# Performance work log

Hardware: AMD Instinct MI355X
Metric: run time of the kernel (lower is better)

Reference implementation:

```python
import jax, jax.numpy as jnp
import numpy as np

EPS = 1e-8  # matches PairwiseCosine eps clamp


def setup_inputs() -> dict:
    key = jax.random.key(0)
    k1, k2, k3 = jax.random.split(key, 3)
    B, N, M, D = 8, 2048, 2048, 256
    desc_src = jax.random.normal(k1, (B, N, D), dtype=jnp.float32)
    desc_dst = jax.random.normal(k2, (B, M, D), dtype=jnp.float32)
    points_dst = jax.random.uniform(k3, (B, M, 2), dtype=jnp.float32)
    return {"desc_src": desc_src, "desc_dst": desc_dst, "points_dst": points_dst}


def reference(desc_src, desc_dst, points_dst):
    # Pairwise cosine similarity: [B, N, M]
    xx = jnp.linalg.norm(desc_src, axis=-1, keepdims=True)          # [B, N, 1]
    yy = jnp.linalg.norm(desc_dst, axis=-1, keepdims=True)          # [B, M, 1]
    xy = jnp.einsum('bnd,bmd->bnm', desc_src, desc_dst)             # [B, N, M]
    sim = xy / jnp.maximum(xx * jnp.swapaxes(yy, 1, 2), EPS)
    # Best match per source descriptor
    confidence = jnp.max(sim, axis=2)                               # [B, N]
    idx = jnp.argmax(sim, axis=2)                                   # [B, N]
    # Gather matched destination points: [B, N, 2]
    matched = jnp.take_along_axis(points_dst, idx[:, :, None], axis=1)
    return (matched, confidence)
```

## Files before the change

kernel.cpp:

```cpp
#include <hip/hip_runtime.h>
#include <stdint.h>

constexpr int Bq = 8, Nq = 2048, Mq = 2048, Dq = 256;
constexpr int TILE = 128;
constexpr int KC = 32;
constexpr int NCH = Dq / KC;
constexpr int LDS_S = 40;

typedef float f32x4 __attribute__((ext_vector_type(4)));
typedef _Float16 f16x8 __attribute__((ext_vector_type(8)));
typedef __fp16 fp16x2 __attribute__((ext_vector_type(2)));

__device__ __forceinline__ uint32_t f2sortable(float f) {
  uint32_t u = __float_as_uint(f);
  return (u & 0x80000000u) ? ~u : (u | 0x80000000u);
}
__device__ __forceinline__ float sortable2f(uint32_t s) {
  uint32_t u = (s & 0x80000000u) ? (s ^ 0x80000000u) : ~s;
  return __uint_as_float(u);
}

__device__ __forceinline__ void load16(float* d, const float* __restrict__ p) {
  *(float4*)&d[0]  = *(const float4*)(p + 0);
  *(float4*)&d[4]  = *(const float4*)(p + 4);
  *(float4*)&d[8]  = *(const float4*)(p + 8);
  *(float4*)&d[12] = *(const float4*)(p + 12);
}

__device__ __forceinline__ void split8(const float* x, f16x8* hi, f16x8* lo,
                                       float& sq) {
  union { f16x8 v; fp16x2 p[4]; } H, L;
#pragma unroll
  for (int j = 0; j < 4; ++j) {
    float x0 = x[2 * j], x1 = x[2 * j + 1];
    sq = fmaf(x0, x0, sq);
    sq = fmaf(x1, x1, sq);
    float h0 = __uint_as_float(__float_as_uint(x0) & 0xFFFFE000u);
    float h1 = __uint_as_float(__float_as_uint(x1) & 0xFFFFE000u);
    H.p[j] = __builtin_amdgcn_cvt_pkrtz(h0, h1);
    L.p[j] = __builtin_amdgcn_cvt_pkrtz(x0 - h0, x1 - h1);
  }
  *hi = H.v;
  *lo = L.v;
}

__global__ __launch_bounds__(256, 3)
void simmax_kernel(const float* __restrict__ src, const float* __restrict__ dst,
                   unsigned long long* __restrict__ best) {
  __shared__ _Float16 Ah[TILE][LDS_S], Al[TILE][LDS_S];
  __shared__ _Float16 Bh[TILE][LDS_S], Bl[TILE][LDS_S];
  __shared__ float invnx_s[TILE], invny_s[TILE];

  const int b = blockIdx.z, nt = blockIdx.y, mt = blockIdx.x;
  const int tid = threadIdx.x;
  const int lane = tid & 63;
  const int wave = tid >> 6;
  const int wy = wave >> 1, wx = wave & 1;
  const int ln15 = lane & 15, lq = lane >> 4;

  const int sr = tid >> 1;
  const int sk = (tid & 1) * 16;
  const float* Ag = src + ((size_t)(b * Nq + nt * TILE + sr)) * Dq + sk;
  const float* Bg = dst + ((size_t)(b * Mq + mt * TILE + sr)) * Dq + sk;

  f32x4 acc[4][4];
#pragma unroll
  for (int i = 0; i < 4; ++i)
#pragma unroll
    for (int j = 0; j < 4; ++j) acc[i][j] = (f32x4){0.f, 0.f, 0.f, 0.f};
  float sqa = 0.f, sqb = 0.f;

  float av[16], bv[16];
  load16(av, Ag);
  load16(bv, Bg);

  for (int c = 0; c < NCH; ++c) {
    f16x8 ah2[2], al2[2], bh2[2], bl2[2];
    split8(&av[0], &ah2[0], &al2[0], sqa);
    split8(&av[8], &ah2[1], &al2[1], sqa);
    split8(&bv[0], &bh2[0], &bl2[0], sqb);
    split8(&bv[8], &bh2[1], &bl2[1], sqb);
    __syncthreads();
    *(f16x8*)&Ah[sr][sk]     = ah2[0];
    *(f16x8*)&Ah[sr][sk + 8] = ah2[1];
    *(f16x8*)&Al[sr][sk]     = al2[0];
    *(f16x8*)&Al[sr][sk + 8] = al2[1];
    *(f16x8*)&Bh[sr][sk]     = bh2[0];
    *(f16x8*)&Bh[sr][sk + 8] = bh2[1];
    *(f16x8*)&Bl[sr][sk]     = bl2[0];
    *(f16x8*)&Bl[sr][sk + 8] = bl2[1];
    __syncthreads();

    if (c + 1 < NCH) {
      load16(av, Ag + (c + 1) * KC);
      load16(bv, Bg + (c + 1) * KC);
    }

    f16x8 bhf[4], blf[4];
#pragma unroll
    for (int ct = 0; ct < 4; ++ct) {
      int rowb = wx * 64 + ct * 16 + ln15;
      bhf[ct] = *(const f16x8*)&Bh[rowb][lq * 8];
      blf[ct] = *(const f16x8*)&Bl[rowb][lq * 8];
    }
#pragma unroll
    for (int rt = 0; rt < 4; ++rt) {
      int rowa = wy * 64 + rt * 16 + ln15;
      f16x8 ahf = *(const f16x8*)&Ah[rowa][lq * 8];
      f16x8 alf = *(const f16x8*)&Al[rowa][lq * 8];
#pragma unroll
      for (int ct = 0; ct < 4; ++ct) {
        acc[rt][ct] = __builtin_amdgcn_mfma_f32_16x16x32_f16(ahf, bhf[ct], acc[rt][ct], 0, 0, 0);
        acc[rt][ct] = __builtin_amdgcn_mfma_f32_16x16x32_f16(ahf, blf[ct], acc[rt][ct], 0, 0, 0);
        acc[rt][ct] = __builtin_amdgcn_mfma_f32_16x16x32_f16(alf, bhf[ct], acc[rt][ct], 0, 0, 0);
      }
    }
  }

  sqa += __shfl_xor(sqa, 1);
  sqb += __shfl_xor(sqb, 1);
  if ((tid & 1) == 0) {
    invnx_s[sr] = 1.0f / sqrtf(sqa);
    invny_s[sr] = 1.0f / sqrtf(sqb);
  }
  __syncthreads();

  float invny[4];
#pragma unroll
  for (int ct = 0; ct < 4; ++ct) invny[ct] = invny_s[wx * 64 + ct * 16 + ln15];

#pragma unroll
  for (int rt = 0; rt < 4; ++rt) {
#pragma unroll
    for (int reg = 0; reg < 4; ++reg) {
      float bq = -1e30f;
      int bc = 0x7FFFFFFF;
#pragma unroll
      for (int ct = 0; ct < 4; ++ct) {
        float q = acc[rt][ct][reg] * invny[ct];
        int cg = mt * TILE + wx * 64 + ct * 16 + ln15;
        if (q > bq || (q == bq && cg < bc)) { bq = q; bc = cg; }
      }
#pragma unroll
      for (int m = 1; m <= 8; m <<= 1) {
        float q2 = __shfl_xor(bq, m);
        int c2 = __shfl_xor(bc, m);
        if (q2 > bq || (q2 == bq && c2 < bc)) { bq = q2; bc = c2; }
      }
      if (ln15 == 0) {
        int rloc = wy * 64 + rt * 16 + lq * 4 + reg;
        float conf = bq * invnx_s[rloc];
        unsigned long long p =
            ((unsigned long long)(f2sortable(conf) ^ 0x80000000u) << 32) |
            (uint32_t)(~(uint32_t)bc);
        atomicMax((long long*)&best[(size_t)b * Nq + nt * TILE + rloc],
                  (long long)p);
      }
    }
  }
}

__global__ void finalize_kernel(const unsigned long long* __restrict__ best,
                                const float* __restrict__ pts,
                                float* __restrict__ out) {
  int i = blockIdx.x * blockDim.x + threadIdx.x;
  if (i >= Bq * Nq) return;
  unsigned long long p = best[i];
  uint32_t s = (uint32_t)(p >> 32) ^ 0x80000000u;
  int idx = (int)(~(uint32_t)(p & 0xFFFFFFFFull));
  float conf = sortable2f(s);
  int b = i / Nq;
  const float* q = pts + ((size_t)b * Mq + (size_t)idx) * 2;
  out[(size_t)i * 2 + 0] = q[0];
  out[(size_t)i * 2 + 1] = q[1];
  out[(size_t)(Bq * Nq) * 2 + i] = conf;
}

extern "C" void kernel_launch(void* const* d_in, const int* in_sizes, int n_in,
                              void* d_out, int out_size, void* d_ws, size_t ws_size,
                              hipStream_t stream) {
  const float* src = (const float*)d_in[0];
  const float* dst = (const float*)d_in[1];
  const float* pts = (const float*)d_in[2];
  float* out = (float*)d_out;

  unsigned long long* best = (unsigned long long*)d_ws;

  {
    dim3 grid(Mq / TILE, Nq / TILE, Bq);
    simmax_kernel<<<grid, 256, 0, stream>>>(src, dst, best);
  }
  {
    int blocks = (Bq * Nq + 255) / 256;
    finalize_kernel<<<blocks, 256, 0, stream>>>(best, pts, out);
  }
}
```

Measured before the change: 149.1 us.

## Precompute fp16 hi/lo splits and norms in a prep pass, stage via global_load_lds

Adds a prep kernel that splits src and dst into fp16 hi/lo halves, computes inverse norms, and writes them in a chunk-major layout. The main MFMA kernel then streams the pre-split tiles straight into double-buffered LDS with global_load_lds, so each tile no longer repeats the split and the sync-heavy register-to-LDS store. This costs an extra kernel launch and a round trip of the fp16 workspace through memory, and the fast path only runs when the workspace is large enough.

```diff
diff --git a/kernel.cpp b/kernel.cpp
--- a/kernel.cpp
+++ b/kernel.cpp
@@ -9,6 +9,7 @@
 
 typedef float f32x4 __attribute__((ext_vector_type(4)));
 typedef _Float16 f16x8 __attribute__((ext_vector_type(8)));
+typedef _Float16 f16x4 __attribute__((ext_vector_type(4)));
 typedef __fp16 fp16x2 __attribute__((ext_vector_type(2)));
 
 __device__ __forceinline__ uint32_t f2sortable(float f) {
@@ -42,6 +43,151 @@
   }
   *hi = H.v;
   *lo = L.v;
+}
+
+
+__global__ __launch_bounds__(256)
+void prep_kernel(const float* __restrict__ src, const float* __restrict__ dst,
+                 _Float16* __restrict__ Ah, _Float16* __restrict__ Al,
+                 _Float16* __restrict__ Bh, _Float16* __restrict__ Bl,
+                 float* __restrict__ invnx, float* __restrict__ invny) {
+  const int lane = threadIdx.x & 63;
+  const int wv = threadIdx.x >> 6;
+  const int r = blockIdx.x * 4 + wv;
+
+  const float* x;
+  _Float16 *h, *l;
+  float* inv;
+  if (blockIdx.y == 0) { x = src; h = Ah; l = Al; inv = invnx; }
+  else                 { x = dst; h = Bh; l = Bl; inv = invny; }
+
+  float4 v = *(const float4*)(x + (size_t)r * Dq + lane * 4);
+  float sq = 0.f;
+  union { f16x4 v; fp16x2 p[2]; } H, L;
+  float e[4] = {v.x, v.y, v.z, v.w};
+#pragma unroll
+  for (int j = 0; j < 2; ++j) {
+    float x0 = e[2 * j], x1 = e[2 * j + 1];
+    sq = fmaf(x0, x0, sq);
+    sq = fmaf(x1, x1, sq);
+    float h0 = __uint_as_float(__float_as_uint(x0) & 0xFFFFE000u);
+    float h1 = __uint_as_float(__float_as_uint(x1) & 0xFFFFE000u);
+    H.p[j] = __builtin_amdgcn_cvt_pkrtz(h0, h1);
+    L.p[j] = __builtin_amdgcn_cvt_pkrtz(x0 - h0, x1 - h1);
+  }
+#pragma unroll
+  for (int m = 1; m <= 32; m <<= 1) sq += __shfl_xor(sq, m);
+
+  const int b = r >> 11, row = r & 2047;
+  const int c = lane >> 3, ko = (lane & 7) * 4;
+  size_t idx = ((size_t)(b * NCH + c) * 2048 + row) * KC + ko;
+  *(f16x4*)&h[idx] = H.v;
+  *(f16x4*)&l[idx] = L.v;
+  if (lane == 0) inv[r] = 1.0f / sqrtf(sq);
+}
+
+__device__ __forceinline__ void stage(const _Float16* g, _Float16* l, int lane) {
+  const char* gc = (const char*)g + lane * 16;
+  char* lc = (char*)l;
+#pragma unroll
+  for (int i = 0; i < 8; ++i)
+    __builtin_amdgcn_global_load_lds(
+        (const __attribute__((address_space(1))) void*)(gc + i * 1024),
+        (__attribute__((address_space(3))) void*)(lc + i * 1024),
+        16, 0, 0);
+}
+
+__global__ __launch_bounds__(256, 2)
+void simmax_mfma(const _Float16* __restrict__ Ah, const _Float16* __restrict__ Al,
+                 const _Float16* __restrict__ Bh, const _Float16* __restrict__ Bl,
+                 const float* __restrict__ invnx, const float* __restrict__ invny,
+                 unsigned long long* __restrict__ best) {
+  __shared__ __align__(16) _Float16 lds[2][4][TILE][KC];
+
+  const int b = blockIdx.z, nt = blockIdx.y, mt = blockIdx.x;
+  const int tid = threadIdx.x;
+  const int lane = tid & 63;
+  const int wave = tid >> 6;
+  const int wy = wave >> 1, wx = wave & 1;
+  const int ln15 = lane & 15, lq = lane >> 4;
+
+  const _Float16* garr = (wave == 0) ? Ah : (wave == 1) ? Al
+                        : (wave == 2) ? Bh : Bl;
+  const int grow = ((wave < 2) ? nt : mt) * TILE;
+  const _Float16* g0 = garr + ((size_t)(b * NCH) * 2048 + grow) * KC;
+  constexpr size_t CSTR = (size_t)2048 * KC;
+
+  f32x4 acc[4][4];
+#pragma unroll
+  for (int i = 0; i < 4; ++i)
+#pragma unroll
+    for (int j = 0; j < 4; ++j) acc[i][j] = (f32x4){0.f, 0.f, 0.f, 0.f};
+
+  stage(g0, &lds[0][wave][0][0], lane);
+  __syncthreads();
+
+#pragma unroll
+  for (int c = 0; c < NCH; ++c) {
+    const int cb = c & 1;
+    if (c + 1 < NCH)
+      stage(g0 + (size_t)(c + 1) * CSTR, &lds[cb ^ 1][wave][0][0], lane);
+
+    f16x8 bhf[4], blf[4];
+#pragma unroll
+    for (int ct = 0; ct < 4; ++ct) {
+      const int rb = wx * 64 + ct * 16 + ln15;
+      bhf[ct] = *(const f16x8*)&lds[cb][2][rb][lq * 8];
+      blf[ct] = *(const f16x8*)&lds[cb][3][rb][lq * 8];
+    }
+#pragma unroll
+    for (int rt = 0; rt < 4; ++rt) {
+      const int ra = wy * 64 + rt * 16 + ln15;
+      f16x8 ahf = *(const f16x8*)&lds[cb][0][ra][lq * 8];
+      f16x8 alf = *(const f16x8*)&lds[cb][1][ra][lq * 8];
+#pragma unroll
+      for (int ct = 0; ct < 4; ++ct) {
+        acc[rt][ct] = __builtin_amdgcn_mfma_f32_16x16x32_f16(ahf, bhf[ct], acc[rt][ct], 0, 0, 0);
+        acc[rt][ct] = __builtin_amdgcn_mfma_f32_16x16x32_f16(ahf, blf[ct], acc[rt][ct], 0, 0, 0);
+        acc[rt][ct] = __builtin_amdgcn_mfma_f32_16x16x32_f16(alf, bhf[ct], acc[rt][ct], 0, 0, 0);
+      }
+    }
+    if (c + 1 < NCH) __syncthreads();
+  }
+
+  float invy[4];
+#pragma unroll
+  for (int ct = 0; ct < 4; ++ct)
+    invy[ct] = invny[(size_t)b * Mq + mt * TILE + wx * 64 + ct * 16 + ln15];
+
+#pragma unroll
+  for (int rt = 0; rt < 4; ++rt) {
+#pragma unroll
+    for (int reg = 0; reg < 4; ++reg) {
+      float bq = -1e30f;
+      int bc = 0x7FFFFFFF;
+#pragma unroll
+      for (int ct = 0; ct < 4; ++ct) {
+        float q = acc[rt][ct][reg] * invy[ct];
+        int cg = mt * TILE + wx * 64 + ct * 16 + ln15;
+        if (q > bq || (q == bq && cg < bc)) { bq = q; bc = cg; }
+      }
+#pragma unroll
+      for (int m = 1; m <= 8; m <<= 1) {
+        float q2 = __shfl_xor(bq, m);
+        int c2 = __shfl_xor(bc, m);
+        if (q2 > bq || (q2 == bq && c2 < bc)) { bq = q2; bc = c2; }
+      }
+      if (ln15 == 0) {
+        int rloc = wy * 64 + rt * 16 + lq * 4 + reg;
+        float conf = bq * invnx[(size_t)b * Nq + nt * TILE + rloc];
+        unsigned long long p =
+            ((unsigned long long)(f2sortable(conf) ^ 0x80000000u) << 32) |
+            (uint32_t)(~(uint32_t)bc);
+        atomicMax((long long*)&best[(size_t)b * Nq + nt * TILE + rloc],
+                  (long long)p);
+      }
+    }
+  }
 }
 
 __global__ __launch_bounds__(256, 3)
@@ -186,9 +332,27 @@
 
   unsigned long long* best = (unsigned long long*)d_ws;
 
-  {
-    dim3 grid(Mq / TILE, Nq / TILE, Bq);
-    simmax_kernel<<<grid, 256, 0, stream>>>(src, dst, best);
+  constexpr size_t BEST_B = (size_t)Bq * Nq * 8;
+  constexpr size_t HL_B   = (size_t)Bq * 2048 * Dq * 2;
+  constexpr size_t INV_B  = (size_t)Bq * 2048 * 4;
+  constexpr size_t NEED   = BEST_B + 4 * HL_B + 2 * INV_B;
+
+  if (ws_size >= NEED) {
+    uint8_t* w = (uint8_t*)d_ws + BEST_B;
+    _Float16* Ah = (_Float16*)(w);
+    _Float16* Al = (_Float16*)(w + 1 * HL_B);
+    _Float16* Bh = (_Float16*)(w + 2 * HL_B);
+    _Float16* Bl = (_Float16*)(w + 3 * HL_B);
+    float* invnx = (float*)(w + 4 * HL_B);
+    float* invny = (float*)(w + 4 * HL_B + INV_B);
+
+    prep_kernel<<<dim3(4096, 2, 1), 256, 0, stream>>>(src, dst, Ah, Al, Bh, Bl,
+                                                      invnx, invny);
+    simmax_mfma<<<dim3(Mq / TILE, Nq / TILE, Bq), 256, 0, stream>>>(
+        Ah, Al, Bh, Bl, invnx, invny, best);
+  } else {
+    simmax_kernel<<<dim3(Mq / TILE, Nq / TILE, Bq), 256, 0, stream>>>(src, dst,
+                                                                      best);
   }
   {
     int blocks = (Bq * Nq + 255) / 256;
```

After: 176.5 us. 18.4% more time.
